# Optimization experiments

Measured on AMD Instinct MI355X. Metric: run time of the kernel, lower is better.

The kernel has to match this reference:

```python
import jax, jax.numpy as jnp
import numpy as np

EPS = 1e-5


def _gcn_norm(edge_index, N):
    # symmetric GCN normalization with self-loops: D^-1/2 (A+I) D^-1/2
    row, col = edge_index[0], edge_index[1]
    loop = jnp.arange(N, dtype=row.dtype)
    row_f = jnp.concatenate([row, loop])
    col_f = jnp.concatenate([col, loop])
    deg = jax.ops.segment_sum(jnp.ones_like(row_f, dtype=jnp.float32), row_f, num_segments=N)
    dinv = jnp.where(deg > 0, jax.lax.rsqrt(jnp.maximum(deg, 1.0)), 0.0)
    norm = dinv[row_f] * dinv[col_f]  # [E+N]
    return row_f, col_f, norm


def _gcn_conv(h, W, b, row_f, col_f, norm, N):
    h = h @ W  # [N, C_out] small GEMM
    msg = h[col_f] * norm[:, None]  # gather over edges  [E+N, C_out]
    return jax.ops.segment_sum(msg, row_f, num_segments=N) + b


def _bn_eval(h, gamma, beta, mean, var):
    return (h - mean) * jax.lax.rsqrt(var + EPS) * gamma + beta


def setup_inputs() -> dict:
    key = jax.random.key(0)
    ks = jax.random.split(key, 12)
    N, E = 100000, 1600000
    C_in, C_hid, C_out = 64, 64, 64
    x = jax.random.normal(ks[0], (N, C_in), dtype=jnp.float32)
    edge_index = jax.random.randint(ks[1], (2, E), 0, N, dtype=jnp.int32)
    s = 1.0 / np.sqrt(C_hid)
    inp = {
        "x": x,
        "edge_index": edge_index,
        "W1": jax.random.normal(ks[2], (C_in, C_hid), dtype=jnp.float32) * s,
        "b1": jnp.zeros((C_hid,), jnp.float32),
        "g1": jnp.ones((C_hid,), jnp.float32),
        "be1": jnp.zeros((C_hid,), jnp.float32),
        "m1": jax.random.normal(ks[3], (C_hid,), dtype=jnp.float32) * 0.1,
        "v1": jax.random.uniform(ks[4], (C_hid,), minval=0.5, maxval=1.5, dtype=jnp.float32),
        "W2": jax.random.normal(ks[5], (C_hid, C_hid), dtype=jnp.float32) * s,
        "b2": jnp.zeros((C_hid,), jnp.float32),
        "g2": jnp.ones((C_hid,), jnp.float32),
        "be2": jnp.zeros((C_hid,), jnp.float32),
        "m2": jax.random.normal(ks[6], (C_hid,), dtype=jnp.float32) * 0.1,
        "v2": jax.random.uniform(ks[7], (C_hid,), minval=0.5, maxval=1.5, dtype=jnp.float32),
        "W3": jax.random.normal(ks[8], (C_hid, C_out), dtype=jnp.float32) * s,
        "b3": jnp.zeros((C_out,), jnp.float32),
    }
    return inp


def reference(x, edge_index, W1, b1, g1, be1, m1, v1, W2, b2, g2, be2, m2, v2, W3, b3):
    N = x.shape[0]
    row_f, col_f, norm = _gcn_norm(edge_index, N)  # cached=True: computed once
    h = _gcn_conv(x, W1, b1, row_f, col_f, norm, N)
    h = jax.nn.relu(_bn_eval(h, g1, be1, m1, v1))  # dropout off (eval)
    h = _gcn_conv(h, W2, b2, row_f, col_f, norm, N)
    h = jax.nn.relu(_bn_eval(h, g2, be2, m2, v2))
    global_embeddings = h
    hc_predictions = _gcn_conv(global_embeddings, W3, b3, row_f, col_f, norm, N)
    return (global_embeddings, hc_predictions)
```

## Files before the change

### kernel.cpp

```cpp
#include <hip/hip_runtime.h>

typedef __attribute__((ext_vector_type(8))) short bfrag8;
typedef __attribute__((ext_vector_type(4))) float facc4;
typedef __attribute__((ext_vector_type(8))) unsigned short u16x8;

#define CROWS  256
#define NCBMAX 512
#define CAP    8192
#define CHUNK  4096
#define SLACK  772
#define BPITCH (CAP + SLACK)
#define TSH    14
#define NTMAX  8

static __device__ __forceinline__ float bf2f(ushort u) {
    union { unsigned int i; float f; } x;
    x.i = ((unsigned int)u) << 16;
    return x.f;
}
static __device__ __forceinline__ ushort f2bf(float f) {
    union { float f; unsigned int i; } x;
    x.f = f;
    unsigned int r = x.i + 0x7FFFu + ((x.i >> 16) & 1u);
    return (ushort)(r >> 16);
}

__global__ void k_prep(const float* __restrict__ W1, const float* __restrict__ W2,
                       const float* __restrict__ W3,
                       const float* __restrict__ b1, const float* __restrict__ g1,
                       const float* __restrict__ be1, const float* __restrict__ m1,
                       const float* __restrict__ v1,
                       const float* __restrict__ b2, const float* __restrict__ g2,
                       const float* __restrict__ be2, const float* __restrict__ m2,
                       const float* __restrict__ v2,
                       const float* __restrict__ b3,
                       ushort* __restrict__ wp, float* __restrict__ pp) {
    int l = blockIdx.x;
    const float* W = (l == 0) ? W1 : (l == 1) ? W2 : W3;
    ushort* wo = wp + l * 4096;
    for (int idx = threadIdx.x; idx < 4096; idx += blockDim.x) {
        int j = idx & 7, m = (idx >> 3) & 15, quad = (idx >> 7) & 3;
        int ks = (idx >> 9) & 1, c2 = idx >> 10;
        wo[idx] = f2bf(W[(32 * ks + 8 * quad + j) * 64 + c2 * 16 + m]);
    }
    if (threadIdx.x < 64) {
        int ch = threadIdx.x;
        float PS, PH;
        if (l == 0) {
            float sc = g1[ch] * rsqrtf(v1[ch] + 1e-5f);
            PS = sc; PH = be1[ch] - m1[ch] * sc + b1[ch] * sc;
        } else if (l == 1) {
            float sc = g2[ch] * rsqrtf(v2[ch] + 1e-5f);
            PS = sc; PH = be2[ch] - m2[ch] * sc + b2[ch] * sc;
        } else {
            PS = 1.f; PH = b3[ch];
        }
        pp[l * 128 + ch] = PS;
        pp[l * 128 + 64 + ch] = PH;
    }
}


__global__ void k_cinit(int* __restrict__ ccur, int ncb,
                        ushort* __restrict__ ta, ushort* __restrict__ tb, int N) {
    int b = blockIdx.x * blockDim.x + threadIdx.x;
    if (b < ncb) ccur[b] = b * CAP;
    if (blockIdx.x == 0 && threadIdx.x < 64) {
        ta[(size_t)N * 64 + threadIdx.x] = 0;
        tb[(size_t)N * 64 + threadIdx.x] = 0;
    }
}

__global__ void k_part(const int* __restrict__ row, const int* __restrict__ col, int E,
                       int* __restrict__ ccur, int* __restrict__ bkt, int ncb) {
    __shared__ int recs[CHUNK];
    __shared__ unsigned short cbl[CHUNK];
    __shared__ int hist[NCBMAX], lbase[NCBMAX], loff[NCBMAX];
    int tid = threadIdx.x;
    int chunk0 = blockIdx.x * CHUNK;
    for (int i = tid; i < ncb; i += blockDim.x) hist[i] = 0;
    __syncthreads();
    for (int j = tid; j < CHUNK; j += blockDim.x) {
        int e = chunk0 + j;
        if (e < E) {
            int r = row[e];
            int cb = r >> 8;
            recs[j] = ((r & (CROWS - 1)) << 17) | col[e];
            cbl[j] = (unsigned short)cb;
            atomicAdd(&hist[cb], 1);
        } else cbl[j] = 0xFFFF;
    }
    __syncthreads();
    for (int i = tid; i < ncb; i += blockDim.x) {
        int h = hist[i];
        lbase[i] = h ? atomicAdd(&ccur[i], h) : 0;
        loff[i] = 0;
    }
    __syncthreads();
    for (int j = tid; j < CHUNK; j += blockDim.x) {
        unsigned short cb = cbl[j];
        if (cb != 0xFFFF) {
            int p = lbase[cb] + atomicAdd(&loff[cb], 1);
            if (p < (cb + 1) * CAP) bkt[p] = recs[j];
        }
    }
}

__global__ void k_build(const int* __restrict__ bkt, const int* __restrict__ ccur,
                        int* __restrict__ rptr, int* __restrict__ deg,
                        float* __restrict__ dinv, int* __restrict__ cidx, int N) {
    __shared__ int hist4[CROWS * NTMAX];
    __shared__ int cur4[CROWS * NTMAX];
    __shared__ int wstart[CROWS], psum[CROWS], degs[CROWS];
    int tid = threadIdx.x;
    int b = blockIdx.x;
    int lo = b * CROWS;
    int nr = min(CROWS, N - lo);
    int in0 = b * CAP;
    int cntE = min(ccur[b] - in0, CAP);
    int out0 = b * BPITCH;

    for (int i = tid; i < CROWS * NTMAX; i += blockDim.x) hist4[i] = 0;
    __syncthreads();
    for (int i = tid; i < cntE; i += blockDim.x) {
        int v = bkt[in0 + i];
        atomicAdd(&hist4[(v >> 17) * NTMAX + ((v & 0x1FFFF) >> TSH)], 1);
    }
    __syncthreads();
    int d = 0, ep = 0;
    if (tid < CROWS) {
        #pragma unroll
        for (int t = 0; t < NTMAX; t++) d += hist4[tid * NTMAX + t];
        ep = (d + 3) & ~3;
        psum[tid] = ep;
        degs[tid] = d;
    }
    __syncthreads();
    #pragma unroll
    for (int off = 1; off < CROWS; off <<= 1) {
        int t = (tid >= off && tid < CROWS) ? psum[tid - off] : 0;
        __syncthreads();
        if (tid < CROWS) psum[tid] += t;
        __syncthreads();
    }
    if (tid < CROWS) {
        int ws = out0 + psum[tid] - ep;
        wstart[tid] = ws;
        int off = ws;
        #pragma unroll
        for (int t = 0; t < NTMAX; t++) {
            cur4[tid * NTMAX + t] = off;
            off += hist4[tid * NTMAX + t];
        }
        if (tid < nr) {
            rptr[lo + tid] = ws;
            deg[lo + tid] = d;
            dinv[lo + tid] = rsqrtf((float)(d + 1));
        }
    }
    __syncthreads();
    for (int i = tid; i < cntE; i += blockDim.x) {
        int v = bkt[in0 + i];
        int c = v & 0x1FFFF;
        int p = atomicAdd(&cur4[(v >> 17) * NTMAX + (c >> TSH)], 1);
        cidx[p] = c;
    }
    __syncthreads();
    if (tid < nr) {
        int dd = degs[tid];
        int epp = (dd + 3) & ~3;
        for (int j = dd; j < epp; j++) cidx[wstart[tid] + j] = N;
    }
}

__global__ void k_gemm(const float* __restrict__ Hv, const ushort* __restrict__ wq,
                       const float* __restrict__ dinv,
                       ushort* __restrict__ T, int ntiles, int N) {
    int lane = threadIdx.x & 63;
    int wid = (blockIdx.x * blockDim.x + threadIdx.x) >> 6;
    int nw = (gridDim.x * blockDim.x) >> 6;
    int m = lane & 15, quad = lane >> 4;

    bfrag8 bf[2][4];
    #pragma unroll
    for (int s = 0; s < 2; s++)
        #pragma unroll
        for (int c = 0; c < 4; c++)
            bf[s][c] = *(const bfrag8*)(wq +
                (size_t)((((c * 2 + s) * 4 + quad) * 16 + m) * 8));

    for (int t = wid; t < ntiles; t += nw) {
        int nodeA = t * 16 + m;
        if (nodeA >= N) nodeA = N - 1;
        bfrag8 a0, a1;
        const float* arow = Hv + (size_t)nodeA * 64;
        #pragma unroll
        for (int s = 0; s < 2; s++) {
            float4 u0 = *(const float4*)(arow + s * 32 + quad * 8);
            float4 u1 = *(const float4*)(arow + s * 32 + quad * 8 + 4);
            bfrag8 f;
            f[0] = (short)f2bf(u0.x); f[1] = (short)f2bf(u0.y);
            f[2] = (short)f2bf(u0.z); f[3] = (short)f2bf(u0.w);
            f[4] = (short)f2bf(u1.x); f[5] = (short)f2bf(u1.y);
            f[6] = (short)f2bf(u1.z); f[7] = (short)f2bf(u1.w);
            if (s == 0) a0 = f; else a1 = f;
        }
        facc4 acc[4];
        #pragma unroll
        for (int c = 0; c < 4; c++) { acc[c][0]=0.f; acc[c][1]=0.f; acc[c][2]=0.f; acc[c][3]=0.f; }
        #pragma unroll
        for (int c = 0; c < 4; c++) {
            acc[c] = __builtin_amdgcn_mfma_f32_16x16x32_bf16(a0, bf[0][c], acc[c], 0, 0, 0);
            acc[c] = __builtin_amdgcn_mfma_f32_16x16x32_bf16(a1, bf[1][c], acc[c], 0, 0, 0);
        }
        #pragma unroll
        for (int c = 0; c < 4; c++)
            #pragma unroll
            for (int r = 0; r < 4; r++) {
                int node = t * 16 + quad * 4 + r;
                if (node < N)
                    T[(size_t)node * 64 + c * 16 + m] = f2bf(dinv[node] * acc[c][r]);
            }
    }
}

template <bool FUSE>
__global__ void k_aggf(const ushort* __restrict__ T2, const int* __restrict__ rptr,
                       const int* __restrict__ deg, const float* __restrict__ dinv,
                       const int* __restrict__ cidx,
                       const float* __restrict__ pp, int relu,
                       const ushort* __restrict__ wq,
                       float* __restrict__ outf, ushort* __restrict__ Tn, int N) {
    __shared__ ushort lds_h[32][72];

    int tid = threadIdx.x;
    int lane = tid & 63;
    int wl = tid >> 6;
    int grp = lane >> 3;
    int s = lane & 7;
    int loc = wl * 8 + grp;
    int r = blockIdx.x * 32 + loc;
    bool rv = (r < N);

    int start = rv ? rptr[r] : 0;
    int ep = rv ? ((deg[r] + 3) & ~3) : 0;
    float a[8];
    #pragma unroll
    for (int k = 0; k < 8; k++) a[k] = 0.f;
    int i = 0;
    for (; i + 8 <= ep; i += 8) {
        int4 c4 = *(const int4*)(cidx + start + i);
        int4 d4 = *(const int4*)(cidx + start + i + 4);
        u16x8 t0 = *(const u16x8*)(T2 + (size_t)c4.x * 64 + s * 8);
        u16x8 t1 = *(const u16x8*)(T2 + (size_t)c4.y * 64 + s * 8);
        u16x8 t2 = *(const u16x8*)(T2 + (size_t)c4.z * 64 + s * 8);
        u16x8 t3 = *(const u16x8*)(T2 + (size_t)c4.w * 64 + s * 8);
        u16x8 t4 = *(const u16x8*)(T2 + (size_t)d4.x * 64 + s * 8);
        u16x8 t5 = *(const u16x8*)(T2 + (size_t)d4.y * 64 + s * 8);
        u16x8 t6 = *(const u16x8*)(T2 + (size_t)d4.z * 64 + s * 8);
        u16x8 t7 = *(const u16x8*)(T2 + (size_t)d4.w * 64 + s * 8);
        #pragma unroll
        for (int k = 0; k < 8; k++)
            a[k] += ((bf2f(t0[k]) + bf2f(t1[k])) + (bf2f(t2[k]) + bf2f(t3[k]))) +
                    ((bf2f(t4[k]) + bf2f(t5[k])) + (bf2f(t6[k]) + bf2f(t7[k])));
    }
    if (i < ep) {
        int4 c4 = *(const int4*)(cidx + start + i);
        u16x8 t0 = *(const u16x8*)(T2 + (size_t)c4.x * 64 + s * 8);
        u16x8 t1 = *(const u16x8*)(T2 + (size_t)c4.y * 64 + s * 8);
        u16x8 t2 = *(const u16x8*)(T2 + (size_t)c4.z * 64 + s * 8);
        u16x8 t3 = *(const u16x8*)(T2 + (size_t)c4.w * 64 + s * 8);
        #pragma unroll
        for (int k = 0; k < 8; k++)
            a[k] += (bf2f(t0[k]) + bf2f(t1[k])) + (bf2f(t2[k]) + bf2f(t3[k]));
    }

    float4 ps0 = *(const float4*)(pp + s * 8);
    float4 ps1 = *(const float4*)(pp + s * 8 + 4);
    float4 ph0 = *(const float4*)(pp + 64 + s * 8);
    float4 ph1 = *(const float4*)(pp + 64 + s * 8 + 4);
    float PS[8] = {ps0.x, ps0.y, ps0.z, ps0.w, ps1.x, ps1.y, ps1.z, ps1.w};
    float PH[8] = {ph0.x, ph0.y, ph0.z, ph0.w, ph1.x, ph1.y, ph1.z, ph1.w};

    float v[8];
    #pragma unroll
    for (int k = 0; k < 8; k++) v[k] = 0.f;
    if (rv) {
        u16x8 sf = *(const u16x8*)(T2 + (size_t)r * 64 + s * 8);
        float dr = dinv[r];
        #pragma unroll
        for (int k = 0; k < 8; k++) {
            v[k] = dr * (a[k] + bf2f(sf[k])) * PS[k] + PH[k];
            if (relu) v[k] = fmaxf(v[k], 0.f);
        }
        if (outf) {
            *(float4*)(outf + (size_t)r * 64 + s * 8) = make_float4(v[0], v[1], v[2], v[3]);
            *(float4*)(outf + (size_t)r * 64 + s * 8 + 4) = make_float4(v[4], v[5], v[6], v[7]);
        }
    }

    if constexpr (FUSE) {
        u16x8 hv;
        #pragma unroll
        for (int k = 0; k < 8; k++) hv[k] = rv ? f2bf(v[k]) : (ushort)0;
        *(u16x8*)&lds_h[loc][s * 8] = hv;

        int m = lane & 15, quad = lane >> 4;
        int rtile = wl >> 1, chalf = wl & 1;
        bfrag8 bw[2][2];
        #pragma unroll
        for (int ks = 0; ks < 2; ks++)
            #pragma unroll
            for (int c = 0; c < 2; c++)
                bw[ks][c] = *(const bfrag8*)(wq +
                    (size_t)(((((chalf * 2 + c) * 2 + ks) * 4 + quad) * 16 + m) * 8));
        __syncthreads();

        bfrag8 a0 = *(const bfrag8*)&lds_h[rtile * 16 + m][quad * 8];
        bfrag8 a1 = *(const bfrag8*)&lds_h[rtile * 16 + m][32 + quad * 8];
        facc4 acc[2];
        #pragma unroll
        for (int c = 0; c < 2; c++) { acc[c][0]=0.f; acc[c][1]=0.f; acc[c][2]=0.f; acc[c][3]=0.f; }
        #pragma unroll
        for (int c = 0; c < 2; c++) {
            acc[c] = __builtin_amdgcn_mfma_f32_16x16x32_bf16(a0, bw[0][c], acc[c], 0, 0, 0);
            acc[c] = __builtin_amdgcn_mfma_f32_16x16x32_bf16(a1, bw[1][c], acc[c], 0, 0, 0);
        }
        int nodeBase = blockIdx.x * 32 + rtile * 16;
        #pragma unroll
        for (int c = 0; c < 2; c++)
            #pragma unroll
            for (int rr = 0; rr < 4; rr++) {
                int node = nodeBase + quad * 4 + rr;
                if (node < N)
                    Tn[(size_t)node * 64 + (chalf * 2 + c) * 16 + m] =
                        f2bf(dinv[node] * acc[c][rr]);
            }
    }
}


extern "C" void kernel_launch(void* const* d_in, const int* in_sizes, int n_in,
                              void* d_out, int out_size, void* d_ws, size_t ws_size,
                              hipStream_t stream) {
    const float* x  = (const float*)d_in[0];
    const int*   ei = (const int*)d_in[1];
    const float *W1 = (const float*)d_in[2],  *b1 = (const float*)d_in[3];
    const float *g1 = (const float*)d_in[4],  *be1= (const float*)d_in[5];
    const float *m1 = (const float*)d_in[6],  *v1 = (const float*)d_in[7];
    const float *W2 = (const float*)d_in[8],  *b2 = (const float*)d_in[9];
    const float *g2 = (const float*)d_in[10], *be2= (const float*)d_in[11];
    const float *m2 = (const float*)d_in[12], *v2 = (const float*)d_in[13];
    const float *W3 = (const float*)d_in[14], *b3 = (const float*)d_in[15];

    int N = in_sizes[0] / 64;
    int E = in_sizes[1] / 2;
    const int* row = ei;
    const int* col = ei + E;
    int ncb = (N + CROWS - 1) / CROWS;

    char* p = (char*)d_ws;
    auto take = [&](size_t b) -> char* {
        char* q = p;
        p += (b + 255) & ~(size_t)255;
        return q;
    };
    int*    ccur  = (int*)   take((size_t)ncb * 4);
    int*    rptr  = (int*)   take((size_t)N * 4);
    int*    deg   = (int*)   take((size_t)N * 4);
    float*  dinv  = (float*) take((size_t)N * 4);
    ushort* wp    = (ushort*)take((size_t)3 * 4096 * 2);
    float*  pp    = (float*) take((size_t)3 * 128 * 4);
    int*    bkt   = (int*)   take((size_t)ncb * CAP * 4);
    int*    cidx  = (int*)   take((size_t)ncb * BPITCH * 4 + 1024);
    ushort* ta    = (ushort*)take((size_t)(N + 1) * 64 * 2);
    ushort* tb    = (ushort*)take((size_t)(N + 1) * 64 * 2);

    const int TB = 256;
    const int TBP = 1024;
    int nchunks = (E + CHUNK - 1) / CHUNK;
    k_prep <<<3, TB, 0, stream>>>(W1, W2, W3, b1, g1, be1, m1, v1,
                                  b2, g2, be2, m2, v2, b3, wp, pp);
    k_cinit<<<(ncb + TB - 1) / TB, TB, 0, stream>>>(ccur, ncb, ta, tb, N);
    k_part <<<nchunks, TBP, 0, stream>>>(row, col, E, ccur, bkt, ncb);
    k_build<<<ncb, TBP, 0, stream>>>(bkt, ccur, rptr, deg, dinv, cidx, N);

    float* outp = (float*)d_out;
    int ntiles = (N + 15) >> 4;
    int GG = (ntiles + 3) / 4;
    int GA = (N + 31) / 32;

    k_gemm<<<GG, TB, 0, stream>>>(x, wp, dinv, ta, ntiles, N);
    k_aggf<true><<<GA, TB, 0, stream>>>(ta, rptr, deg, dinv, cidx, pp, 1,
                                        wp + 4096, (float*)nullptr, tb, N);
    k_aggf<true><<<GA, TB, 0, stream>>>(tb, rptr, deg, dinv, cidx, pp + 128, 1,
                                        wp + 8192, outp, ta, N);
    k_aggf<false><<<GA, TB, 0, stream>>>(ta, rptr, deg, dinv, cidx, pp + 256, 0,
                                         (const ushort*)nullptr,
                                         outp + (size_t)N * 64, (ushort*)nullptr, N);
}
```

Before: 261.2 us.

## Replace bucketed CSR build with global atomic degree count, scan, and place

```diff
diff --git a/kernel.cpp b/kernel.cpp
--- a/kernel.cpp
+++ b/kernel.cpp
@@ -5,13 +5,8 @@
 typedef __attribute__((ext_vector_type(8))) unsigned short u16x8;
 
 #define CROWS  256
-#define NCBMAX 512
-#define CAP    8192
-#define CHUNK  4096
 #define SLACK  772
-#define BPITCH (CAP + SLACK)
-#define TSH    14
-#define NTMAX  8
+#define BPITCH (8192 + SLACK)
 
 static __device__ __forceinline__ float bf2f(ushort u) {
     union { unsigned int i; float f; } x;
@@ -34,142 +29,87 @@
                        const float* __restrict__ be2, const float* __restrict__ m2,
                        const float* __restrict__ v2,
                        const float* __restrict__ b3,
-                       ushort* __restrict__ wp, float* __restrict__ pp) {
+                       ushort* __restrict__ wp, float* __restrict__ pp,
+                       int* __restrict__ deg,
+                       ushort* __restrict__ ta, ushort* __restrict__ tb, int N) {
     int l = blockIdx.x;
-    const float* W = (l == 0) ? W1 : (l == 1) ? W2 : W3;
-    ushort* wo = wp + l * 4096;
-    for (int idx = threadIdx.x; idx < 4096; idx += blockDim.x) {
-        int j = idx & 7, m = (idx >> 3) & 15, quad = (idx >> 7) & 3;
-        int ks = (idx >> 9) & 1, c2 = idx >> 10;
-        wo[idx] = f2bf(W[(32 * ks + 8 * quad + j) * 64 + c2 * 16 + m]);
-    }
-    if (threadIdx.x < 64) {
-        int ch = threadIdx.x;
-        float PS, PH;
-        if (l == 0) {
-            float sc = g1[ch] * rsqrtf(v1[ch] + 1e-5f);
-            PS = sc; PH = be1[ch] - m1[ch] * sc + b1[ch] * sc;
-        } else if (l == 1) {
-            float sc = g2[ch] * rsqrtf(v2[ch] + 1e-5f);
-            PS = sc; PH = be2[ch] - m2[ch] * sc + b2[ch] * sc;
-        } else {
-            PS = 1.f; PH = b3[ch];
-        }
-        pp[l * 128 + ch] = PS;
-        pp[l * 128 + 64 + ch] = PH;
-    }
-}
-
-
-__global__ void k_cinit(int* __restrict__ ccur, int ncb,
-                        ushort* __restrict__ ta, ushort* __restrict__ tb, int N) {
-    int b = blockIdx.x * blockDim.x + threadIdx.x;
-    if (b < ncb) ccur[b] = b * CAP;
-    if (blockIdx.x == 0 && threadIdx.x < 64) {
-        ta[(size_t)N * 64 + threadIdx.x] = 0;
-        tb[(size_t)N * 64 + threadIdx.x] = 0;
-    }
-}
-
-__global__ void k_part(const int* __restrict__ row, const int* __restrict__ col, int E,
-                       int* __restrict__ ccur, int* __restrict__ bkt, int ncb) {
-    __shared__ int recs[CHUNK];
-    __shared__ unsigned short cbl[CHUNK];
-    __shared__ int hist[NCBMAX], lbase[NCBMAX], loff[NCBMAX];
-    int tid = threadIdx.x;
-    int chunk0 = blockIdx.x * CHUNK;
-    for (int i = tid; i < ncb; i += blockDim.x) hist[i] = 0;
-    __syncthreads();
-    for (int j = tid; j < CHUNK; j += blockDim.x) {
-        int e = chunk0 + j;
-        if (e < E) {
-            int r = row[e];
-            int cb = r >> 8;
-            recs[j] = ((r & (CROWS - 1)) << 17) | col[e];
-            cbl[j] = (unsigned short)cb;
-            atomicAdd(&hist[cb], 1);
-        } else cbl[j] = 0xFFFF;
-    }
-    __syncthreads();
-    for (int i = tid; i < ncb; i += blockDim.x) {
-        int h = hist[i];
-        lbase[i] = h ? atomicAdd(&ccur[i], h) : 0;
-        loff[i] = 0;
-    }
-    __syncthreads();
-    for (int j = tid; j < CHUNK; j += blockDim.x) {
-        unsigned short cb = cbl[j];
-        if (cb != 0xFFFF) {
-            int p = lbase[cb] + atomicAdd(&loff[cb], 1);
-            if (p < (cb + 1) * CAP) bkt[p] = recs[j];
-        }
-    }
-}
-
-__global__ void k_build(const int* __restrict__ bkt, const int* __restrict__ ccur,
-                        int* __restrict__ rptr, int* __restrict__ deg,
-                        float* __restrict__ dinv, int* __restrict__ cidx, int N) {
-    __shared__ int hist4[CROWS * NTMAX];
-    __shared__ int cur4[CROWS * NTMAX];
-    __shared__ int wstart[CROWS], psum[CROWS], degs[CROWS];
+    if (l < 3) {
+        const float* W = (l == 0) ? W1 : (l == 1) ? W2 : W3;
+        ushort* wo = wp + l * 4096;
+        for (int idx = threadIdx.x; idx < 4096; idx += blockDim.x) {
+            int j = idx & 7, m = (idx >> 3) & 15, quad = (idx >> 7) & 3;
+            int ks = (idx >> 9) & 1, c2 = idx >> 10;
+            wo[idx] = f2bf(W[(32 * ks + 8 * quad + j) * 64 + c2 * 16 + m]);
+        }
+        if (threadIdx.x < 64) {
+            int ch = threadIdx.x;
+            float PS, PH;
+            if (l == 0) {
+                float sc = g1[ch] * rsqrtf(v1[ch] + 1e-5f);
+                PS = sc; PH = be1[ch] - m1[ch] * sc + b1[ch] * sc;
+            } else if (l == 1) {
+                float sc = g2[ch] * rsqrtf(v2[ch] + 1e-5f);
+                PS = sc; PH = be2[ch] - m2[ch] * sc + b2[ch] * sc;
+            } else {
+                PS = 1.f; PH = b3[ch];
+            }
+            pp[l * 128 + ch] = PS;
+            pp[l * 128 + 64 + ch] = PH;
+        }
+    }
+    if (l == 3 && threadIdx.x < 128) {
+        int t = threadIdx.x;
+        if (t < 64) ta[(size_t)N * 64 + t] = 0;
+        else        tb[(size_t)N * 64 + (t - 64)] = 0;
+    }
+    int t = blockIdx.x * blockDim.x + threadIdx.x;
+    int stride = gridDim.x * blockDim.x;
+    for (int i = t; i < N; i += stride) deg[i] = 0;
+}
+
+
+__global__ void k_deg(const int* __restrict__ row, int E, int* __restrict__ deg) {
+    int t = blockIdx.x * blockDim.x + threadIdx.x;
+    int stride = gridDim.x * blockDim.x;
+    for (int e = t; e < E; e += stride) atomicAdd(&deg[row[e]], 1);
+}
+
+__global__ void k_scanB(const int* __restrict__ deg, int* __restrict__ rptr,
+                        float* __restrict__ dinv, int* __restrict__ cur,
+                        int* __restrict__ cidx, int N) {
+    __shared__ int psum[CROWS];
     int tid = threadIdx.x;
     int b = blockIdx.x;
     int lo = b * CROWS;
     int nr = min(CROWS, N - lo);
-    int in0 = b * CAP;
-    int cntE = min(ccur[b] - in0, CAP);
-    int out0 = b * BPITCH;
-
-    for (int i = tid; i < CROWS * NTMAX; i += blockDim.x) hist4[i] = 0;
-    __syncthreads();
-    for (int i = tid; i < cntE; i += blockDim.x) {
-        int v = bkt[in0 + i];
-        atomicAdd(&hist4[(v >> 17) * NTMAX + ((v & 0x1FFFF) >> TSH)], 1);
-    }
-    __syncthreads();
-    int d = 0, ep = 0;
-    if (tid < CROWS) {
-        #pragma unroll
-        for (int t = 0; t < NTMAX; t++) d += hist4[tid * NTMAX + t];
-        ep = (d + 3) & ~3;
-        psum[tid] = ep;
-        degs[tid] = d;
-    }
+    int d = (tid < nr) ? deg[lo + tid] : 0;
+    int ep = (d + 3) & ~3;
+    psum[tid] = ep;
     __syncthreads();
     #pragma unroll
     for (int off = 1; off < CROWS; off <<= 1) {
-        int t = (tid >= off && tid < CROWS) ? psum[tid - off] : 0;
+        int t = (tid >= off) ? psum[tid - off] : 0;
         __syncthreads();
-        if (tid < CROWS) psum[tid] += t;
+        psum[tid] += t;
         __syncthreads();
     }
-    if (tid < CROWS) {
-        int ws = out0 + psum[tid] - ep;
-        wstart[tid] = ws;
-        int off = ws;
-        #pragma unroll
-        for (int t = 0; t < NTMAX; t++) {
-            cur4[tid * NTMAX + t] = off;
-            off += hist4[tid * NTMAX + t];
-        }
-        if (tid < nr) {
-            rptr[lo + tid] = ws;
-            deg[lo + tid] = d;
-            dinv[lo + tid] = rsqrtf((float)(d + 1));
-        }
-    }
-    __syncthreads();
-    for (int i = tid; i < cntE; i += blockDim.x) {
-        int v = bkt[in0 + i];
-        int c = v & 0x1FFFF;
-        int p = atomicAdd(&cur4[(v >> 17) * NTMAX + (c >> TSH)], 1);
-        cidx[p] = c;
-    }
-    __syncthreads();
     if (tid < nr) {
-        int dd = degs[tid];
-        int epp = (dd + 3) & ~3;
-        for (int j = dd; j < epp; j++) cidx[wstart[tid] + j] = N;
+        int ws = b * BPITCH + psum[tid] - ep;
+        rptr[lo + tid] = ws;
+        cur[lo + tid] = ws;
+        dinv[lo + tid] = rsqrtf((float)(d + 1));
+        for (int j = d; j < ep; j++) cidx[ws + j] = N;
+    }
+}
+
+__global__ void k_place(const int* __restrict__ row, const int* __restrict__ col, int E,
+                        int* __restrict__ cur, int* __restrict__ cidx) {
+    int t = blockIdx.x * blockDim.x + threadIdx.x;
+    int stride = gridDim.x * blockDim.x;
+    for (int e = t; e < E; e += stride) {
+        int r = row[e];
+        int p = atomicAdd(&cur[r], 1);
+        cidx[p] = col[e];
     }
 }
 
@@ -225,12 +165,13 @@
 }
 
 template <bool FUSE>
-__global__ void k_aggf(const ushort* __restrict__ T2, const int* __restrict__ rptr,
-                       const int* __restrict__ deg, const float* __restrict__ dinv,
-                       const int* __restrict__ cidx,
-                       const float* __restrict__ pp, int relu,
-                       const ushort* __restrict__ wq,
-                       float* __restrict__ outf, ushort* __restrict__ Tn, int N) {
+__global__ void __launch_bounds__(256, 6)
+k_aggf(const ushort* __restrict__ T2, const int* __restrict__ rptr,
+       const int* __restrict__ deg, const float* __restrict__ dinv,
+       const int* __restrict__ cidx,
+       const float* __restrict__ pp, int relu,
+       const ushort* __restrict__ wq,
+       float* __restrict__ outf, ushort* __restrict__ Tn, int N) {
     __shared__ ushort lds_h[32][72];
 
     int tid = threadIdx.x;
@@ -241,16 +182,32 @@
     int loc = wl * 8 + grp;
     int r = blockIdx.x * 32 + loc;
     bool rv = (r < N);
+    int rs = rv ? r : N;
 
     int start = rv ? rptr[r] : 0;
     int ep = rv ? ((deg[r] + 3) & ~3) : 0;
+    u16x8 sf = *(const u16x8*)(T2 + (size_t)rs * 64 + s * 8);
+    float dr = rv ? dinv[r] : 0.f;
+
     float a[8];
     #pragma unroll
     for (int k = 0; k < 8; k++) a[k] = 0.f;
+
     int i = 0;
-    for (; i + 8 <= ep; i += 8) {
-        int4 c4 = *(const int4*)(cidx + start + i);
-        int4 d4 = *(const int4*)(cidx + start + i + 4);
+    bool have8 = (8 <= ep);
+    int4 c4, d4;
+    if (have8) {
+        c4 = *(const int4*)(cidx + start);
+        d4 = *(const int4*)(cidx + start + 4);
+    }
+    while (have8) {
+        int ni = i + 8;
+        bool nhave = (ni + 8 <= ep);
+        int4 nc4, nd4;
+        if (nhave) {
+            nc4 = *(const int4*)(cidx + start + ni);
+            nd4 = *(const int4*)(cidx + start + ni + 4);
+        }
         u16x8 t0 = *(const u16x8*)(T2 + (size_t)c4.x * 64 + s * 8);
         u16x8 t1 = *(const u16x8*)(T2 + (size_t)c4.y * 64 + s * 8);
         u16x8 t2 = *(const u16x8*)(T2 + (size_t)c4.z * 64 + s * 8);
@@ -263,13 +220,14 @@
         for (int k = 0; k < 8; k++)
             a[k] += ((bf2f(t0[k]) + bf2f(t1[k])) + (bf2f(t2[k]) + bf2f(t3[k]))) +
                     ((bf2f(t4[k]) + bf2f(t5[k])) + (bf2f(t6[k]) + bf2f(t7[k])));
+        c4 = nc4; d4 = nd4; i = ni; have8 = nhave;
     }
     if (i < ep) {
-        int4 c4 = *(const int4*)(cidx + start + i);
-        u16x8 t0 = *(const u16x8*)(T2 + (size_t)c4.x * 64 + s * 8);
-        u16x8 t1 = *(const u16x8*)(T2 + (size_t)c4.y * 64 + s * 8);
-        u16x8 t2 = *(const u16x8*)(T2 + (size_t)c4.z * 64 + s * 8);
-        u16x8 t3 = *(const u16x8*)(T2 + (size_t)c4.w * 64 + s * 8);
+        int4 e4 = *(const int4*)(cidx + start + i);
+        u16x8 t0 = *(const u16x8*)(T2 + (size_t)e4.x * 64 + s * 8);
+        u16x8 t1 = *(const u16x8*)(T2 + (size_t)e4.y * 64 + s * 8);
+        u16x8 t2 = *(const u16x8*)(T2 + (size_t)e4.z * 64 + s * 8);
+        u16x8 t3 = *(const u16x8*)(T2 + (size_t)e4.w * 64 + s * 8);
         #pragma unroll
         for (int k = 0; k < 8; k++)
             a[k] += (bf2f(t0[k]) + bf2f(t1[k])) + (bf2f(t2[k]) + bf2f(t3[k]));
@@ -286,8 +244,6 @@
     #pragma unroll
     for (int k = 0; k < 8; k++) v[k] = 0.f;
     if (rv) {
-        u16x8 sf = *(const u16x8*)(T2 + (size_t)r * 64 + s * 8);
-        float dr = dinv[r];
         #pragma unroll
         for (int k = 0; k < 8; k++) {
             v[k] = dr * (a[k] + bf2f(sf[k])) * PS[k] + PH[k];
@@ -365,25 +321,25 @@
         p += (b + 255) & ~(size_t)255;
         return q;
     };
-    int*    ccur  = (int*)   take((size_t)ncb * 4);
     int*    rptr  = (int*)   take((size_t)N * 4);
     int*    deg   = (int*)   take((size_t)N * 4);
+    int*    cur   = (int*)   take((size_t)N * 4);
     float*  dinv  = (float*) take((size_t)N * 4);
     ushort* wp    = (ushort*)take((size_t)3 * 4096 * 2);
     float*  pp    = (float*) take((size_t)3 * 128 * 4);
-    int*    bkt   = (int*)   take((size_t)ncb * CAP * 4);
     int*    cidx  = (int*)   take((size_t)ncb * BPITCH * 4 + 1024);
     ushort* ta    = (ushort*)take((size_t)(N + 1) * 64 * 2);
     ushort* tb    = (ushort*)take((size_t)(N + 1) * 64 * 2);
 
     const int TB = 256;
     const int TBP = 1024;
-    int nchunks = (E + CHUNK - 1) / CHUNK;
-    k_prep <<<3, TB, 0, stream>>>(W1, W2, W3, b1, g1, be1, m1, v1,
-                                  b2, g2, be2, m2, v2, b3, wp, pp);
-    k_cinit<<<(ncb + TB - 1) / TB, TB, 0, stream>>>(ccur, ncb, ta, tb, N);
-    k_part <<<nchunks, TBP, 0, stream>>>(row, col, E, ccur, bkt, ncb);
-    k_build<<<ncb, TBP, 0, stream>>>(bkt, ccur, rptr, deg, dinv, cidx, N);
+    int GE = (E + TBP * 4 - 1) / (TBP * 4);
+
+    k_prep <<<32, TB, 0, stream>>>(W1, W2, W3, b1, g1, be1, m1, v1,
+                                   b2, g2, be2, m2, v2, b3, wp, pp, deg, ta, tb, N);
+    k_deg  <<<GE, TBP, 0, stream>>>(row, E, deg);
+    k_scanB<<<ncb, CROWS, 0, stream>>>(deg, rptr, dinv, cur, cidx, N);
+    k_place<<<GE, TBP, 0, stream>>>(row, col, E, cur, cidx);
 
     float* outp = (float*)d_out;
     int ntiles = (N + 15) >> 4;
```

Measured after the change: 402.6 us. 54.1% more time.

## Drop column-tiled CSR sort, prefetch neighbor indices, bound aggf occupancy

Applied to the files above, without the earlier changes.

```diff
diff --git a/kernel.cpp b/kernel.cpp
--- a/kernel.cpp
+++ b/kernel.cpp
@@ -10,8 +10,6 @@
 #define CHUNK  4096
 #define SLACK  772
 #define BPITCH (CAP + SLACK)
-#define TSH    14
-#define NTMAX  8
 
 static __device__ __forceinline__ float bf2f(ushort u) {
     union { unsigned int i; float f; } x;
@@ -109,9 +107,7 @@
 __global__ void k_build(const int* __restrict__ bkt, const int* __restrict__ ccur,
                         int* __restrict__ rptr, int* __restrict__ deg,
                         float* __restrict__ dinv, int* __restrict__ cidx, int N) {
-    __shared__ int hist4[CROWS * NTMAX];
-    __shared__ int cur4[CROWS * NTMAX];
-    __shared__ int wstart[CROWS], psum[CROWS], degs[CROWS];
+    __shared__ int hist[CROWS], wstart[CROWS], cur[CROWS], psum[CROWS];
     int tid = threadIdx.x;
     int b = blockIdx.x;
     int lo = b * CROWS;
@@ -120,20 +116,16 @@
     int cntE = min(ccur[b] - in0, CAP);
     int out0 = b * BPITCH;
 
-    for (int i = tid; i < CROWS * NTMAX; i += blockDim.x) hist4[i] = 0;
-    __syncthreads();
-    for (int i = tid; i < cntE; i += blockDim.x) {
-        int v = bkt[in0 + i];
-        atomicAdd(&hist4[(v >> 17) * NTMAX + ((v & 0x1FFFF) >> TSH)], 1);
-    }
+    if (tid < CROWS) hist[tid] = 0;
+    __syncthreads();
+    for (int i = tid; i < cntE; i += blockDim.x)
+        atomicAdd(&hist[bkt[in0 + i] >> 17], 1);
     __syncthreads();
     int d = 0, ep = 0;
     if (tid < CROWS) {
-        #pragma unroll
-        for (int t = 0; t < NTMAX; t++) d += hist4[tid * NTMAX + t];
+        d = hist[tid];
         ep = (d + 3) & ~3;
         psum[tid] = ep;
-        degs[tid] = d;
     }
     __syncthreads();
     #pragma unroll
@@ -146,12 +138,7 @@
     if (tid < CROWS) {
         int ws = out0 + psum[tid] - ep;
         wstart[tid] = ws;
-        int off = ws;
-        #pragma unroll
-        for (int t = 0; t < NTMAX; t++) {
-            cur4[tid * NTMAX + t] = off;
-            off += hist4[tid * NTMAX + t];
-        }
+        cur[tid] = ws;
         if (tid < nr) {
             rptr[lo + tid] = ws;
             deg[lo + tid] = d;
@@ -161,13 +148,12 @@
     __syncthreads();
     for (int i = tid; i < cntE; i += blockDim.x) {
         int v = bkt[in0 + i];
-        int c = v & 0x1FFFF;
-        int p = atomicAdd(&cur4[(v >> 17) * NTMAX + (c >> TSH)], 1);
-        cidx[p] = c;
+        int p = atomicAdd(&cur[v >> 17], 1);
+        cidx[p] = v & 0x1FFFF;
     }
     __syncthreads();
     if (tid < nr) {
-        int dd = degs[tid];
+        int dd = hist[tid];
         int epp = (dd + 3) & ~3;
         for (int j = dd; j < epp; j++) cidx[wstart[tid] + j] = N;
     }
@@ -225,12 +211,13 @@
 }
 
 template <bool FUSE>
-__global__ void k_aggf(const ushort* __restrict__ T2, const int* __restrict__ rptr,
-                       const int* __restrict__ deg, const float* __restrict__ dinv,
-                       const int* __restrict__ cidx,
-                       const float* __restrict__ pp, int relu,
-                       const ushort* __restrict__ wq,
-                       float* __restrict__ outf, ushort* __restrict__ Tn, int N) {
+__global__ void __launch_bounds__(256, 6)
+k_aggf(const ushort* __restrict__ T2, const int* __restrict__ rptr,
+       const int* __restrict__ deg, const float* __restrict__ dinv,
+       const int* __restrict__ cidx,
+       const float* __restrict__ pp, int relu,
+       const ushort* __restrict__ wq,
+       float* __restrict__ outf, ushort* __restrict__ Tn, int N) {
     __shared__ ushort lds_h[32][72];
 
     int tid = threadIdx.x;
@@ -241,16 +228,32 @@
     int loc = wl * 8 + grp;
     int r = blockIdx.x * 32 + loc;
     bool rv = (r < N);
+    int rs = rv ? r : N;
 
     int start = rv ? rptr[r] : 0;
     int ep = rv ? ((deg[r] + 3) & ~3) : 0;
+    u16x8 sf = *(const u16x8*)(T2 + (size_t)rs * 64 + s * 8);
+    float dr = rv ? dinv[r] : 0.f;
+
     float a[8];
     #pragma unroll
     for (int k = 0; k < 8; k++) a[k] = 0.f;
+
     int i = 0;
-    for (; i + 8 <= ep; i += 8) {
-        int4 c4 = *(const int4*)(cidx + start + i);
-        int4 d4 = *(const int4*)(cidx + start + i + 4);
+    bool have8 = (8 <= ep);
+    int4 c4, d4;
+    if (have8) {
+        c4 = *(const int4*)(cidx + start);
+        d4 = *(const int4*)(cidx + start + 4);
+    }
+    while (have8) {
+        int ni = i + 8;
+        bool nhave = (ni + 8 <= ep);
+        int4 nc4, nd4;
+        if (nhave) {
+            nc4 = *(const int4*)(cidx + start + ni);
+            nd4 = *(const int4*)(cidx + start + ni + 4);
+        }
         u16x8 t0 = *(const u16x8*)(T2 + (size_t)c4.x * 64 + s * 8);
         u16x8 t1 = *(const u16x8*)(T2 + (size_t)c4.y * 64 + s * 8);
         u16x8 t2 = *(const u16x8*)(T2 + (size_t)c4.z * 64 + s * 8);
@@ -263,13 +266,14 @@
         for (int k = 0; k < 8; k++)
             a[k] += ((bf2f(t0[k]) + bf2f(t1[k])) + (bf2f(t2[k]) + bf2f(t3[k]))) +
                     ((bf2f(t4[k]) + bf2f(t5[k])) + (bf2f(t6[k]) + bf2f(t7[k])));
+        c4 = nc4; d4 = nd4; i = ni; have8 = nhave;
     }
     if (i < ep) {
-        int4 c4 = *(const int4*)(cidx + start + i);
-        u16x8 t0 = *(const u16x8*)(T2 + (size_t)c4.x * 64 + s * 8);
-        u16x8 t1 = *(const u16x8*)(T2 + (size_t)c4.y * 64 + s * 8);
-        u16x8 t2 = *(const u16x8*)(T2 + (size_t)c4.z * 64 + s * 8);
-        u16x8 t3 = *(const u16x8*)(T2 + (size_t)c4.w * 64 + s * 8);
+        int4 e4 = *(const int4*)(cidx + start + i);
+        u16x8 t0 = *(const u16x8*)(T2 + (size_t)e4.x * 64 + s * 8);
+        u16x8 t1 = *(const u16x8*)(T2 + (size_t)e4.y * 64 + s * 8);
+        u16x8 t2 = *(const u16x8*)(T2 + (size_t)e4.z * 64 + s * 8);
+        u16x8 t3 = *(const u16x8*)(T2 + (size_t)e4.w * 64 + s * 8);
         #pragma unroll
         for (int k = 0; k < 8; k++)
             a[k] += (bf2f(t0[k]) + bf2f(t1[k])) + (bf2f(t2[k]) + bf2f(t3[k]));
@@ -286,8 +290,6 @@
     #pragma unroll
     for (int k = 0; k < 8; k++) v[k] = 0.f;
     if (rv) {
-        u16x8 sf = *(const u16x8*)(T2 + (size_t)r * 64 + s * 8);
-        float dr = dinv[r];
         #pragma unroll
         for (int k = 0; k < 8; k++) {
             v[k] = dr * (a[k] + bf2f(sf[k])) * PS[k] + PH[k];
```

Result: no change. 258.9 us (-0.9%).
